# Performance work log

Hardware: AMD Instinct MI355X
Metric: run time of the kernel (lower is better)

Reference implementation:

```python
import jax, jax.numpy as jnp
import numpy as np

B = 4096
INPUT_DIM = 4096
N_BLOCKS = 8
BLOCK = INPUT_DIM // N_BLOCKS  # 512
N_EXPERTS = 6
H = 1024   # expert_hidden
H2 = H // 2


def setup_inputs() -> dict:
    key = jax.random.key(0)
    ks = jax.random.split(key, 16)
    s = 0.02  # init scale keeps tanh/softmax in sane range
    return {
        "x":   jax.random.normal(ks[0], (B, INPUT_DIM), jnp.float32),
        # routers: per-block stacked weights [8, ...]
        "Wr1": jax.random.normal(ks[1], (N_BLOCKS, BLOCK, 32), jnp.float32) * s,
        "br1": jax.random.normal(ks[2], (N_BLOCKS, 32), jnp.float32) * s,
        "Wr2": jax.random.normal(ks[3], (N_BLOCKS, 32, N_EXPERTS), jnp.float32) * s,
        "br2": jax.random.normal(ks[4], (N_BLOCKS, N_EXPERTS), jnp.float32) * s,
        # experts: stacked [6, ...], shared across all 8 blocks
        "We1": jax.random.normal(ks[5], (N_EXPERTS, BLOCK, H), jnp.float32) * s,
        "be1": jax.random.normal(ks[6], (N_EXPERTS, H), jnp.float32) * s,
        "We2": jax.random.normal(ks[7], (N_EXPERTS, H, H2), jnp.float32) * s,
        "be2": jax.random.normal(ks[8], (N_EXPERTS, H2), jnp.float32) * s,
        "We3": jax.random.normal(ks[9], (N_EXPERTS, H2, 3), jnp.float32) * s,
        "be3": jax.random.normal(ks[10], (N_EXPERTS, 3), jnp.float32) * s,
        # aggregator
        "Wa1": jax.random.normal(ks[11], (3, 16), jnp.float32) * s,
        "ba1": jax.random.normal(ks[12], (16,), jnp.float32) * s,
        "Wa2": jax.random.normal(ks[13], (16, 3), jnp.float32) * s,
        "ba2": jax.random.normal(ks[14], (3,), jnp.float32) * s,
    }


def reference(x, Wr1, br1, Wr2, br2, We1, be1, We2, be2, We3, be3,
              Wa1, ba1, Wa2, ba2):
    b = x.shape[0]
    blocks = x.reshape(b, N_BLOCKS, BLOCK)                       # [b,s,d]
    # routers (one per block s)
    r1 = jax.nn.relu(jnp.einsum('bsd,sdh->bsh', blocks, Wr1) + br1)
    routing = jax.nn.softmax(
        jnp.einsum('bsh,she->bse', r1, Wr2) + br2, axis=-1)      # [b,s,E]
    # experts applied to every block (grouped GEMMs)
    h1 = jnp.tanh(jnp.einsum('bsd,edh->bseh', blocks, We1) + be1)        # [b,s,E,H]
    h2 = jnp.tanh(jnp.einsum('bseh,ehk->bsek', h1, We2) + be2)           # [b,s,E,H2]
    eo = jnp.einsum('bsek,eko->bseo', h2, We3) + be3                     # [b,s,E,3]
    weighted = jnp.einsum('bse,bseo->bso', routing, eo)                  # [b,s,3]
    final = weighted.mean(axis=1)                                        # mean over 8 blocks
    a1 = jax.nn.relu(final @ Wa1 + ba1)
    return a1 @ Wa2 + ba2                                                # [b,3]
```

## Files before the change

kernel.cpp:

```cpp
#include <hip/hip_runtime.h>
#include <cstdint>
#include <cstddef>

typedef __bf16 bf16;
typedef __bf16 bf16x4 __attribute__((ext_vector_type(4)));
typedef __bf16 bf16x8 __attribute__((ext_vector_type(8)));
typedef float  f32x4  __attribute__((ext_vector_type(4)));
typedef long long i64v;

#define NROWS   32768
#define DBLK    512
#define H1N     1024
#define H2N     512
#define NEXP    6
#define NBATCH  4096
#define HALL    (NEXP * H1N)
#define W2SCALE 32.0f
#define W2INV   0.03125f

__device__ __forceinline__ void gld16(const void* g, void* l) {
    __builtin_amdgcn_global_load_lds(
        (const __attribute__((address_space(1))) void*)g,
        (__attribute__((address_space(3))) void*)l, 16, 0, 0);
}

__device__ __forceinline__ float fast_tanh(float x) {
    float e = __builtin_amdgcn_exp2f(x * 2.8853900817779268f);
    float r = __builtin_amdgcn_rcpf(e + 1.0f);
    return __builtin_fmaf(-2.0f, r, 1.0f);
}

__device__ __forceinline__ float hsum16(float v) {
    v += __shfl_xor(v, 1);
    v += __shfl_xor(v, 2);
    v += __shfl_xor(v, 4);
    v += __shfl_xor(v, 8);
    return v;
}

__device__ __forceinline__ int swz(int row, int g) {
    return row * 64 + ((g ^ (row & 7)) * 8);
}
__device__ __forceinline__ int swz8(int row, int g) {
    return row * 64 + ((g ^ ((row >> 1) & 3)) << 4);
}


__global__ void cvt_bf16_kernel(const float* __restrict__ in,
                                bf16* __restrict__ out, int n4) {
    int i = blockIdx.x * blockDim.x + threadIdx.x;
    if (i >= n4) return;
    float4 v = ((const float4*)in)[i];
    bf16x4 o;
    o.x = (bf16)v.x; o.y = (bf16)v.y; o.z = (bf16)v.z; o.w = (bf16)v.w;
    ((bf16x4*)out)[i] = o;
}

__global__ __launch_bounds__(256) void transpose_cvt(
    const float* __restrict__ in, bf16* __restrict__ out, int K, int N) {
    __shared__ bf16 tile[64][66];
    int e  = blockIdx.z;
    int n0 = blockIdx.x * 64;
    int k0 = blockIdx.y * 64;
    int c  = threadIdx.x & 63;
    int rb = threadIdx.x >> 6;
    const float* src = in + (size_t)e * K * N;
    bf16* dst = out + (size_t)e * N * K;
#pragma unroll
    for (int it = 0; it < 16; ++it) {
        int k = k0 + rb + it * 4;
        int n = n0 + c;
        if (k < K && n < N) tile[rb + it * 4][c] = (bf16)src[(size_t)k * N + n];
    }
    __syncthreads();
#pragma unroll
    for (int it = 0; it < 16; ++it) {
        int n = n0 + rb + it * 4;
        int k = k0 + c;
        if (n < N && k < K) dst[(size_t)n * K + k] = tile[c][rb + it * 4];
    }
}

__global__ __launch_bounds__(256) void transpose_cvt_fp8(
    const float* __restrict__ in, uint8_t* __restrict__ out, int K, int N,
    float scale) {
    __shared__ float tile[64][65];
    int e  = blockIdx.z;
    int n0 = blockIdx.x * 64;
    int k0 = blockIdx.y * 64;
    int c  = threadIdx.x & 63;
    int rb = threadIdx.x >> 6;
    const float* src = in + (size_t)e * K * N;
    uint8_t* dst = out + (size_t)e * N * K;
#pragma unroll
    for (int it = 0; it < 16; ++it) {
        int k = k0 + rb + it * 4;
        int n = n0 + c;
        if (k < K && n < N) tile[rb + it * 4][c] = src[(size_t)k * N + n];
    }
    __syncthreads();
#pragma unroll
    for (int it = 0; it < 16; ++it) {
        int n = n0 + rb + it * 4;
        int k = k0 + c;
        if (n < N && k < K) {
            float v = tile[c][rb + it * 4] * scale;
            int p = __builtin_amdgcn_cvt_pk_fp8_f32(v, v, 0, false);
            dst[(size_t)n * K + k] = (uint8_t)(p & 0xff);
        }
    }
}

__global__ void zero_f32_kernel(float* __restrict__ p, int n) {
    int i = blockIdx.x * blockDim.x + threadIdx.x;
    if (i < n) p[i] = 0.0f;
}


__global__ __launch_bounds__(256, 2) void router_kernel(
    const bf16* __restrict__ xbf,
    const bf16* __restrict__ Wr1t,
    const float* __restrict__ br1,
    const float* __restrict__ Wr2,
    const float* __restrict__ br2,
    float* __restrict__ routing) {
    __shared__ __align__(16) bf16 sA[128 * 64];
    __shared__ __align__(16) bf16 sB[32 * 64];
    const int tid = threadIdx.x;
    const int w = tid >> 6, l = tid & 63;
    const int s  = blockIdx.y;
    const int b0 = blockIdx.x * 128;
    const int wm = w * 32;
    const int srow = l >> 3, schk = (l & 7) * 8;
    const int fr = l & 15, fq = l >> 4;
    const bf16* Ab = xbf + (size_t)s * 512;
    const bf16* Bb = Wr1t + (size_t)s * (32 * 512);

    f32x4 acc[2][2];
#pragma unroll
    for (int i = 0; i < 2; ++i)
#pragma unroll
        for (int j = 0; j < 2; ++j) acc[i][j] = (f32x4){0.f, 0.f, 0.f, 0.f};

    for (int k0 = 0; k0 < 512; k0 += 64) {
        __syncthreads();
#pragma unroll
        for (int jj = 0; jj < 4; ++jj) {
            int row = w * 32 + jj * 8;
            gld16(Ab + (size_t)(b0 + row + srow) * 4096 + k0 + schk, sA + row * 64);
        }
        gld16(Bb + (size_t)(w * 8 + srow) * 512 + k0 + schk, sB + w * 8 * 64);
        __syncthreads();
#pragma unroll
        for (int ks = 0; ks < 2; ++ks) {
            bf16x8 af[2], bfr[2];
#pragma unroll
            for (int i = 0; i < 2; ++i)
                af[i] = *(const bf16x8*)&sA[(wm + i * 16 + fr) * 64 + ks * 32 + fq * 8];
#pragma unroll
            for (int j = 0; j < 2; ++j)
                bfr[j] = *(const bf16x8*)&sB[(j * 16 + fr) * 64 + ks * 32 + fq * 8];
#pragma unroll
            for (int i = 0; i < 2; ++i)
#pragma unroll
                for (int j = 0; j < 2; ++j)
                    acc[i][j] = __builtin_amdgcn_mfma_f32_16x16x32_bf16(
                        af[i], bfr[j], acc[i][j], 0, 0, 0);
        }
    }

    float b1v[2], w2v[2][6], br2v[6];
#pragma unroll
    for (int j = 0; j < 2; ++j) {
        int col = j * 16 + fr;
        b1v[j] = br1[s * 32 + col];
#pragma unroll
        for (int e2 = 0; e2 < 6; ++e2) w2v[j][e2] = Wr2[(s * 32 + col) * 6 + e2];
    }
#pragma unroll
    for (int e2 = 0; e2 < 6; ++e2) br2v[e2] = br2[s * 6 + e2];

#pragma unroll
    for (int i = 0; i < 2; ++i) {
#pragma unroll
        for (int r = 0; r < 4; ++r) {
            float lg[6] = {0.f, 0.f, 0.f, 0.f, 0.f, 0.f};
#pragma unroll
            for (int j = 0; j < 2; ++j) {
                float t = fmaxf(acc[i][j][r] + b1v[j], 0.f);
#pragma unroll
                for (int e2 = 0; e2 < 6; ++e2) lg[e2] += t * w2v[j][e2];
            }
#pragma unroll
            for (int e2 = 0; e2 < 6; ++e2) lg[e2] = hsum16(lg[e2]) + br2v[e2];
            float mx = lg[0];
#pragma unroll
            for (int e2 = 1; e2 < 6; ++e2) mx = fmaxf(mx, lg[e2]);
            float p[6], sum = 0.f;
#pragma unroll
            for (int e2 = 0; e2 < 6; ++e2) { p[e2] = __expf(lg[e2] - mx); sum += p[e2]; }
            float inv = __fdividef(1.f, sum);
            if (fr == 0) {
                int brow = b0 + wm + i * 16 + fq * 4 + r;
                float* dst = routing + ((size_t)brow * 8 + s) * 6;
#pragma unroll
                for (int e2 = 0; e2 < 6; ++e2) dst[e2] = p[e2] * inv;
            }
        }
    }
}

__global__ __launch_bounds__(512, 2) void gemm1_kernel(
    const bf16* __restrict__ A,
    const bf16* __restrict__ B,
    const float* __restrict__ bias,
    uint8_t* __restrict__ h1,
    int ldh) {
    __shared__ __align__(16) bf16 sA[2][256 * 64];
    __shared__ __align__(16) bf16 sB[2][256 * 64];
    const int tid = threadIdx.x;
    const int w = tid >> 6, l = tid & 63;
    const int n0 = blockIdx.x * 256;
    const int m0 = blockIdx.y * 256;
    const int wm = (w & 1) * 128;
    const int wn = (w >> 1) * 64;
    const int srow = l >> 3;
    const int gcol = ((l & 7) ^ srow) * 8;
    const int fr = l & 15, fq = l >> 4;

    f32x4 acc[8][4];
#pragma unroll
    for (int i = 0; i < 8; ++i)
#pragma unroll
        for (int j = 0; j < 4; ++j) acc[i][j] = (f32x4){0.f, 0.f, 0.f, 0.f};

    const bf16* Abase = A + (size_t)(m0 + w * 32 + srow) * DBLK + gcol;
    const bf16* Bbase = B + (size_t)(n0 + w * 32 + srow) * DBLK + gcol;

#pragma unroll
    for (int jj = 0; jj < 4; ++jj) {
        gld16(Abase + (size_t)(jj * 8) * DBLK, &sA[0][(w * 32 + jj * 8) * 64]);
        gld16(Bbase + (size_t)(jj * 8) * DBLK, &sB[0][(w * 32 + jj * 8) * 64]);
    }

    for (int t = 0; t < 7; ++t) {
        const int nb = (t + 1) & 1, cb = t & 1;
        const int k1 = (t + 1) * 64;
#pragma unroll
        for (int jj = 0; jj < 4; ++jj) {
            gld16(Abase + (size_t)(jj * 8) * DBLK + k1, &sA[nb][(w * 32 + jj * 8) * 64]);
            gld16(Bbase + (size_t)(jj * 8) * DBLK + k1, &sB[nb][(w * 32 + jj * 8) * 64]);
        }
        asm volatile("s_waitcnt vmcnt(8)" ::: "memory");
        __builtin_amdgcn_s_barrier();
        __builtin_amdgcn_sched_barrier(0);
#pragma unroll
        for (int ks = 0; ks < 2; ++ks) {
            bf16x8 af[8], bfr[4];
#pragma unroll
            for (int i = 0; i < 8; ++i)
                af[i] = *(const bf16x8*)&sA[cb][swz(wm + i * 16 + fr, ks * 4 + fq)];
#pragma unroll
            for (int j = 0; j < 4; ++j)
                bfr[j] = *(const bf16x8*)&sB[cb][swz(wn + j * 16 + fr, ks * 4 + fq)];
#pragma unroll
            for (int i = 0; i < 8; ++i)
#pragma unroll
                for (int j = 0; j < 4; ++j)
                    acc[i][j] = __builtin_amdgcn_mfma_f32_16x16x32_bf16(
                        af[i], bfr[j], acc[i][j], 0, 0, 0);
        }
        asm volatile("" ::: "memory");
        __builtin_amdgcn_s_barrier();
        __builtin_amdgcn_sched_barrier(0);
    }
    asm volatile("s_waitcnt vmcnt(0)" ::: "memory");
    __builtin_amdgcn_s_barrier();
    __builtin_amdgcn_sched_barrier(0);
#pragma unroll
    for (int ks = 0; ks < 2; ++ks) {
        bf16x8 af[8], bfr[4];
#pragma unroll
        for (int i = 0; i < 8; ++i)
            af[i] = *(const bf16x8*)&sA[1][swz(wm + i * 16 + fr, ks * 4 + fq)];
#pragma unroll
        for (int j = 0; j < 4; ++j)
            bfr[j] = *(const bf16x8*)&sB[1][swz(wn + j * 16 + fr, ks * 4 + fq)];
#pragma unroll
        for (int i = 0; i < 8; ++i)
#pragma unroll
            for (int j = 0; j < 4; ++j)
                acc[i][j] = __builtin_amdgcn_mfma_f32_16x16x32_bf16(
                    af[i], bfr[j], acc[i][j], 0, 0, 0);
    }

#pragma unroll
    for (int i = 0; i < 8; ++i) {
        int colb = m0 + wm + i * 16 + fq * 4;
        float4 bb = *(const float4*)&bias[colb];
#pragma unroll
        for (int j = 0; j < 4; ++j) {
            int xrow = n0 + wn + j * 16 + fr;
            float t0 = fast_tanh(acc[i][j][0] + bb.x);
            float t1 = fast_tanh(acc[i][j][1] + bb.y);
            float t2 = fast_tanh(acc[i][j][2] + bb.z);
            float t3 = fast_tanh(acc[i][j][3] + bb.w);
            int p = 0;
            p = __builtin_amdgcn_cvt_pk_fp8_f32(t0, t1, p, false);
            p = __builtin_amdgcn_cvt_pk_fp8_f32(t2, t3, p, true);
            *(uint32_t*)&h1[(size_t)xrow * ldh + colb] = (uint32_t)p;
        }
    }
}

__global__ __launch_bounds__(256, 4) void gemm2_kernel(
    const uint8_t* __restrict__ h1,
    const uint8_t* __restrict__ W2f8t,
    const float* __restrict__ be2,
    const float* __restrict__ We3,
    float* __restrict__ eo,
    int ldh) {
    __shared__ __align__(16) uint8_t sA[128 * 64];
    __shared__ __align__(16) uint8_t sB[128 * 64];
    __shared__ float w3s[128 * 3];
    __shared__ float b2s[128];
    const int tid = threadIdx.x;
    const int w = tid >> 6, l = tid & 63;
    const int e  = blockIdx.z;
    const int n0 = blockIdx.x * 128;
    const int m0 = blockIdx.y * 128;
    const int wm = (w & 1) * 64, wn = (w >> 1) * 64;
    const int srow4 = l >> 2;
    const int g4 = (((l & 3) ^ ((l >> 3) & 3)) << 4);
    const int fr = l & 15, fq = l >> 4;
    const uint8_t* Ae = W2f8t + (size_t)e * (H2N * H1N);
    const uint8_t* Be = h1 + (size_t)e * H1N;

    if (tid < 128) {
        int c = m0 + tid;
        b2s[tid] = be2[e * H2N + c];
        w3s[tid * 3 + 0] = We3[((size_t)e * H2N + c) * 3 + 0];
        w3s[tid * 3 + 1] = We3[((size_t)e * H2N + c) * 3 + 1];
        w3s[tid * 3 + 2] = We3[((size_t)e * H2N + c) * 3 + 2];
    }

    f32x4 acc[4][4];
#pragma unroll
    for (int i = 0; i < 4; ++i)
#pragma unroll
        for (int j = 0; j < 4; ++j) acc[i][j] = (f32x4){0.f, 0.f, 0.f, 0.f};

    for (int k0 = 0; k0 < H1N; k0 += 64) {
        __syncthreads();
#pragma unroll
        for (int jj = 0; jj < 2; ++jj) {
            int row = w * 32 + jj * 16 + srow4;
            gld16(Ae + (size_t)(m0 + row) * H1N + k0 + g4, sA + (w * 32 + jj * 16) * 64);
            gld16(Be + (size_t)(n0 + row) * ldh + k0 + g4, sB + (w * 32 + jj * 16) * 64);
        }
        __syncthreads();
#pragma unroll
        for (int ks = 0; ks < 2; ++ks) {
            i64v af[4], bfr[4];
#pragma unroll
            for (int i = 0; i < 4; ++i) {
                int row = wm + i * 16 + fr;
                af[i] = *(const i64v*)&sA[swz8(row, ks * 2 + (fq >> 1)) + ((fq & 1) << 3)];
            }
#pragma unroll
            for (int j = 0; j < 4; ++j) {
                int row = wn + j * 16 + fr;
                bfr[j] = *(const i64v*)&sB[swz8(row, ks * 2 + (fq >> 1)) + ((fq & 1) << 3)];
            }
#pragma unroll
            for (int i = 0; i < 4; ++i)
#pragma unroll
                for (int j = 0; j < 4; ++j)
                    acc[i][j] = __builtin_amdgcn_mfma_f32_16x16x32_fp8_fp8(
                        af[i], bfr[j], acc[i][j], 0, 0, 0);
        }
    }

    float p[4][3];
#pragma unroll
    for (int j = 0; j < 4; ++j) { p[j][0] = 0.f; p[j][1] = 0.f; p[j][2] = 0.f; }
#pragma unroll
    for (int i = 0; i < 4; ++i) {
        int cl = wm + i * 16 + fq * 4;
        float4 bb = *(const float4*)&b2s[cl];
        float4 wa = *(const float4*)&w3s[cl * 3 + 0];
        float4 wb = *(const float4*)&w3s[cl * 3 + 4];
        float4 wc = *(const float4*)&w3s[cl * 3 + 8];
        float bias4[4] = {bb.x, bb.y, bb.z, bb.w};
        float w30[4] = {wa.x, wa.w, wb.z, wc.y};
        float w31[4] = {wa.y, wb.x, wb.w, wc.z};
        float w32[4] = {wa.z, wb.y, wc.x, wc.w};
#pragma unroll
        for (int j = 0; j < 4; ++j) {
#pragma unroll
            for (int r = 0; r < 4; ++r) {
                float t = fast_tanh(acc[i][j][r] * W2INV + bias4[r]);
                p[j][0] += t * w30[r];
                p[j][1] += t * w31[r];
                p[j][2] += t * w32[r];
            }
        }
    }
#pragma unroll
    for (int j = 0; j < 4; ++j) {
        float v0 = p[j][0], v1 = p[j][1], v2 = p[j][2];
        v0 += __shfl_xor(v0, 16); v0 += __shfl_xor(v0, 32);
        v1 += __shfl_xor(v1, 16); v1 += __shfl_xor(v1, 32);
        v2 += __shfl_xor(v2, 16); v2 += __shfl_xor(v2, 32);
        if (fq == 0) {
            int xrow = n0 + wn + j * 16 + fr;
            float* dst = eo + ((size_t)e * NROWS + xrow) * 3;
            atomicAdd(dst + 0, v0);
            atomicAdd(dst + 1, v1);
            atomicAdd(dst + 2, v2);
        }
    }
}

__global__ void final_kernel(
    const float* __restrict__ routing, const float* __restrict__ eo,
    const float* __restrict__ be3, const float* __restrict__ Wa1,
    const float* __restrict__ ba1, const float* __restrict__ Wa2,
    const float* __restrict__ ba2, float* __restrict__ out) {
    int b = blockIdx.x * blockDim.x + threadIdx.x;
    if (b >= NBATCH) return;
    float f0 = 0.f, f1 = 0.f, f2 = 0.f;
    for (int s = 0; s < 8; ++s) {
        int r = b * 8 + s;
        const float* rt = routing + (size_t)r * 6;
#pragma unroll
        for (int e = 0; e < 6; ++e) {
            float wgt = rt[e];
            const float* eop = eo + ((size_t)e * NROWS + r) * 3;
            f0 += wgt * (eop[0] + be3[e * 3 + 0]);
            f1 += wgt * (eop[1] + be3[e * 3 + 1]);
            f2 += wgt * (eop[2] + be3[e * 3 + 2]);
        }
    }
    f0 *= 0.125f; f1 *= 0.125f; f2 *= 0.125f;
    float o0 = ba2[0], o1 = ba2[1], o2 = ba2[2];
#pragma unroll
    for (int h = 0; h < 16; ++h) {
        float a = f0 * Wa1[h] + f1 * Wa1[16 + h] + f2 * Wa1[32 + h] + ba1[h];
        a = fmaxf(a, 0.f);
        o0 += a * Wa2[h * 3 + 0];
        o1 += a * Wa2[h * 3 + 1];
        o2 += a * Wa2[h * 3 + 2];
    }
    out[b * 3 + 0] = o0;
    out[b * 3 + 1] = o1;
    out[b * 3 + 2] = o2;
}


extern "C" void kernel_launch(void* const* d_in, const int* in_sizes, int n_in,
                              void* d_out, int out_size, void* d_ws, size_t ws_size,
                              hipStream_t stream) {
    const float* x   = (const float*)d_in[0];
    const float* Wr1 = (const float*)d_in[1];
    const float* br1 = (const float*)d_in[2];
    const float* Wr2 = (const float*)d_in[3];
    const float* br2 = (const float*)d_in[4];
    const float* We1 = (const float*)d_in[5];
    const float* be1 = (const float*)d_in[6];
    const float* We2 = (const float*)d_in[7];
    const float* be2 = (const float*)d_in[8];
    const float* We3 = (const float*)d_in[9];
    const float* be3 = (const float*)d_in[10];
    const float* Wa1 = (const float*)d_in[11];
    const float* ba1 = (const float*)d_in[12];
    const float* Wa2 = (const float*)d_in[13];
    const float* ba2 = (const float*)d_in[14];
    float* out = (float*)d_out;

    char* ws = (char*)d_ws;
    const size_t off_xbf  = 0;
    const size_t off_w1t  = off_xbf  + (size_t)33554432;
    const size_t off_w2t  = off_w1t  + (size_t)6291456;
    const size_t off_wr1t = off_w2t  + (size_t)6291456;
    const size_t off_rout = off_wr1t + (size_t)262144;
    const size_t off_eo   = off_rout + (size_t)786432;
    const size_t off_h1   = off_eo   + (size_t)2359296;

    if (off_h1 + (size_t)NROWS * HALL > ws_size) return;

    bf16*    xbf     = (bf16*)(ws + off_xbf);
    bf16*    W1t     = (bf16*)(ws + off_w1t);
    uint8_t* W2f8t   = (uint8_t*)(ws + off_w2t);
    bf16*    Wr1t    = (bf16*)(ws + off_wr1t);
    float*   routing = (float*)(ws + off_rout);
    float*   eo      = (float*)(ws + off_eo);
    uint8_t* h1      = (uint8_t*)(ws + off_h1);

    cvt_bf16_kernel<<<16384, 256, 0, stream>>>(x, xbf, 4194304);
    transpose_cvt<<<dim3(16, 8, 6), 256, 0, stream>>>(We1, W1t, 512, 1024);
    transpose_cvt_fp8<<<dim3(8, 16, 6), 256, 0, stream>>>(We2, W2f8t, 1024, 512, W2SCALE);
    transpose_cvt<<<dim3(1, 8, 8), 256, 0, stream>>>(Wr1, Wr1t, 512, 32);
    zero_f32_kernel<<<2304, 256, 0, stream>>>(eo, 589824);

    router_kernel<<<dim3(32, 8), 256, 0, stream>>>(xbf, Wr1t, br1, Wr2, br2, routing);

    gemm1_kernel<<<dim3(NROWS / 256, HALL / 256), 512, 0, stream>>>(
        W1t, xbf, be1, h1, HALL);
    gemm2_kernel<<<dim3(NROWS / 128, H2N / 128, NEXP), 256, 0, stream>>>(
        h1, W2f8t, be2, We3, eo, HALL);

    final_kernel<<<16, 256, 0, stream>>>(routing, eo, be3, Wa1, ba1, Wa2, ba2, out);
}
```

Measured before the change: 621.2 us.

## Use 4-stage K=32 LDS pipeline with single barrier and swizzled block order in gemm1

After: 690.8 us. 1.11x slower.

```diff
diff --git a/kernel.cpp b/kernel.cpp
--- a/kernel.cpp
+++ b/kernel.cpp
@@ -38,9 +38,6 @@
     return v;
 }
 
-__device__ __forceinline__ int swz(int row, int g) {
-    return row * 64 + ((g ^ (row & 7)) * 8);
-}
 __device__ __forceinline__ int swz8(int row, int g) {
     return row * 64 + ((g ^ ((row >> 1) & 3)) << 4);
 }
@@ -216,99 +213,114 @@
     const float* __restrict__ bias,
     uint8_t* __restrict__ h1,
     int ldh) {
-    __shared__ __align__(16) bf16 sA[2][256 * 64];
-    __shared__ __align__(16) bf16 sB[2][256 * 64];
+    __shared__ __align__(16) bf16 sA[4][256 * 32];
+    __shared__ __align__(16) bf16 sB[4][256 * 32];
     const int tid = threadIdx.x;
     const int w = tid >> 6, l = tid & 63;
-    const int n0 = blockIdx.x * 256;
-    const int m0 = blockIdx.y * 256;
+    const int bid = blockIdx.y * 128 + blockIdx.x;
+    const int nid = (bid & 7) * 384 + (bid >> 3);
+    const int n0 = (nid & 127) * 256;
+    const int m0 = (nid >> 7) * 256;
     const int wm = (w & 1) * 128;
     const int wn = (w >> 1) * 64;
-    const int srow = l >> 3;
-    const int gcol = ((l & 7) ^ srow) * 8;
     const int fr = l & 15, fq = l >> 4;
 
+    const int srow = l >> 2;
+    const int dg   = l & 3;
+    const int lrow0 = w * 32 + srow;
+    const int lrow1 = w * 32 + 16 + srow;
+    const int sg0 = dg ^ ((lrow0 >> 1) & 3);
+    const int sg1 = dg ^ ((lrow1 >> 1) & 3);
+    const bf16* Asrc0 = A + (size_t)(m0 + lrow0) * DBLK + sg0 * 8;
+    const bf16* Asrc1 = A + (size_t)(m0 + lrow1) * DBLK + sg1 * 8;
+    const bf16* Bsrc0 = B + (size_t)(n0 + lrow0) * DBLK + sg0 * 8;
+    const bf16* Bsrc1 = B + (size_t)(n0 + lrow1) * DBLK + sg1 * 8;
+    const int ldsA0 = (w * 32) * 32;
+    const int ldsA1 = (w * 32 + 16) * 32;
+
+    int aoff[8], boff[4];
+#pragma unroll
+    for (int i = 0; i < 8; ++i) {
+        int r = wm + i * 16 + fr;
+        aoff[i] = r * 32 + ((fq ^ ((r >> 1) & 3)) * 8);
+    }
+#pragma unroll
+    for (int j = 0; j < 4; ++j) {
+        int r = wn + j * 16 + fr;
+        boff[j] = r * 32 + ((fq ^ ((r >> 1) & 3)) * 8);
+    }
+
     f32x4 acc[8][4];
 #pragma unroll
     for (int i = 0; i < 8; ++i)
 #pragma unroll
         for (int j = 0; j < 4; ++j) acc[i][j] = (f32x4){0.f, 0.f, 0.f, 0.f};
 
-    const bf16* Abase = A + (size_t)(m0 + w * 32 + srow) * DBLK + gcol;
-    const bf16* Bbase = B + (size_t)(n0 + w * 32 + srow) * DBLK + gcol;
-
-#pragma unroll
-    for (int jj = 0; jj < 4; ++jj) {
-        gld16(Abase + (size_t)(jj * 8) * DBLK, &sA[0][(w * 32 + jj * 8) * 64]);
-        gld16(Bbase + (size_t)(jj * 8) * DBLK, &sB[0][(w * 32 + jj * 8) * 64]);
-    }
-
-    for (int t = 0; t < 7; ++t) {
-        const int nb = (t + 1) & 1, cb = t & 1;
-        const int k1 = (t + 1) * 64;
-#pragma unroll
-        for (int jj = 0; jj < 4; ++jj) {
-            gld16(Abase + (size_t)(jj * 8) * DBLK + k1, &sA[nb][(w * 32 + jj * 8) * 64]);
-            gld16(Bbase + (size_t)(jj * 8) * DBLK + k1, &sB[nb][(w * 32 + jj * 8) * 64]);
-        }
-        asm volatile("s_waitcnt vmcnt(8)" ::: "memory");
-        __builtin_amdgcn_s_barrier();
-        __builtin_amdgcn_sched_barrier(0);
-#pragma unroll
-        for (int ks = 0; ks < 2; ++ks) {
-            bf16x8 af[8], bfr[4];
-#pragma unroll
-            for (int i = 0; i < 8; ++i)
-                af[i] = *(const bf16x8*)&sA[cb][swz(wm + i * 16 + fr, ks * 4 + fq)];
-#pragma unroll
-            for (int j = 0; j < 4; ++j)
-                bfr[j] = *(const bf16x8*)&sB[cb][swz(wn + j * 16 + fr, ks * 4 + fq)];
-#pragma unroll
-            for (int i = 0; i < 8; ++i)
-#pragma unroll
-                for (int j = 0; j < 4; ++j)
-                    acc[i][j] = __builtin_amdgcn_mfma_f32_16x16x32_bf16(
-                        af[i], bfr[j], acc[i][j], 0, 0, 0);
-        }
-        asm volatile("" ::: "memory");
-        __builtin_amdgcn_s_barrier();
-        __builtin_amdgcn_sched_barrier(0);
-    }
-    asm volatile("s_waitcnt vmcnt(0)" ::: "memory");
+#pragma unroll
+    for (int s = 0; s < 3; ++s) {
+        gld16(Asrc0 + s * 32, &sA[s][ldsA0]);
+        gld16(Asrc1 + s * 32, &sA[s][ldsA1]);
+        gld16(Bsrc0 + s * 32, &sB[s][ldsA0]);
+        gld16(Bsrc1 + s * 32, &sB[s][ldsA1]);
+    }
+    asm volatile("s_waitcnt vmcnt(8)" ::: "memory");
     __builtin_amdgcn_s_barrier();
     __builtin_amdgcn_sched_barrier(0);
-#pragma unroll
-    for (int ks = 0; ks < 2; ++ks) {
+
+#pragma unroll
+    for (int t = 0; t < 16; ++t) {
+        const int sl = t & 3;
         bf16x8 af[8], bfr[4];
 #pragma unroll
         for (int i = 0; i < 8; ++i)
-            af[i] = *(const bf16x8*)&sA[1][swz(wm + i * 16 + fr, ks * 4 + fq)];
+            af[i] = *(const bf16x8*)&sA[sl][aoff[i]];
 #pragma unroll
         for (int j = 0; j < 4; ++j)
-            bfr[j] = *(const bf16x8*)&sB[1][swz(wn + j * 16 + fr, ks * 4 + fq)];
+            bfr[j] = *(const bf16x8*)&sB[sl][boff[j]];
+        if (t < 13) {
+            const int s2 = (t + 3) & 3;
+            const int ko = (t + 3) * 32;
+            gld16(Asrc0 + ko, &sA[s2][ldsA0]);
+            gld16(Asrc1 + ko, &sA[s2][ldsA1]);
+            gld16(Bsrc0 + ko, &sB[s2][ldsA0]);
+            gld16(Bsrc1 + ko, &sB[s2][ldsA1]);
+            asm volatile("s_waitcnt vmcnt(8)" ::: "memory");
+        } else if (t == 13) {
+            asm volatile("s_waitcnt vmcnt(4)" ::: "memory");
+        } else {
+            asm volatile("s_waitcnt vmcnt(0)" ::: "memory");
+        }
+        __builtin_amdgcn_sched_barrier(0);
+        __builtin_amdgcn_s_setprio(1);
 #pragma unroll
         for (int i = 0; i < 8; ++i)
 #pragma unroll
             for (int j = 0; j < 4; ++j)
                 acc[i][j] = __builtin_amdgcn_mfma_f32_16x16x32_bf16(
                     af[i], bfr[j], acc[i][j], 0, 0, 0);
-    }
-
-#pragma unroll
-    for (int i = 0; i < 8; ++i) {
-        int colb = m0 + wm + i * 16 + fq * 4;
-        float4 bb = *(const float4*)&bias[colb];
-#pragma unroll
-        for (int j = 0; j < 4; ++j) {
-            int xrow = n0 + wn + j * 16 + fr;
-            float t0 = fast_tanh(acc[i][j][0] + bb.x);
-            float t1 = fast_tanh(acc[i][j][1] + bb.y);
-            float t2 = fast_tanh(acc[i][j][2] + bb.z);
-            float t3 = fast_tanh(acc[i][j][3] + bb.w);
+        __builtin_amdgcn_s_setprio(0);
+        __builtin_amdgcn_s_barrier();
+        __builtin_amdgcn_sched_barrier(0);
+    }
+
+    float4 bb[8];
+#pragma unroll
+    for (int i = 0; i < 8; ++i)
+        bb[i] = *(const float4*)&bias[m0 + wm + i * 16 + fq * 4];
+#pragma unroll
+    for (int j = 0; j < 4; ++j) {
+        int xrow = n0 + wn + j * 16 + fr;
+        uint8_t* dst = &h1[(size_t)xrow * ldh + m0 + wm + fq * 4];
+#pragma unroll
+        for (int i = 0; i < 8; ++i) {
+            float t0 = fast_tanh(acc[i][j][0] + bb[i].x);
+            float t1 = fast_tanh(acc[i][j][1] + bb[i].y);
+            float t2 = fast_tanh(acc[i][j][2] + bb[i].z);
+            float t3 = fast_tanh(acc[i][j][3] + bb[i].w);
             int p = 0;
             p = __builtin_amdgcn_cvt_pk_fp8_f32(t0, t1, p, false);
             p = __builtin_amdgcn_cvt_pk_fp8_f32(t2, t3, p, true);
-            *(uint32_t*)&h1[(size_t)xrow * ldh + colb] = (uint32_t)p;
+            *(uint32_t*)(dst + i * 16) = (uint32_t)p;
         }
     }
 }
```
